# Kernel optimization log

Hardware: AMD Instinct MI355X
Metric: run time of the kernel (lower is better)

## Reference

```python
import jax, jax.numpy as jnp
import numpy as np

B, L, D, H, TOPO = 2, 1024, 1024, 16, 8
Dh = D // H
N_SLOTS = B * L


def _rope_apply(x, cos, sin):
    # x: [B,H,L,Dh]; cos/sin: [B,1,L,Dh//2]
    x1 = x[..., 0::2]
    x2 = x[..., 1::2]
    y1 = x1 * cos - x2 * sin
    y2 = x1 * sin + x2 * cos
    return jnp.stack([y1, y2], axis=-1).reshape(x.shape)


def setup_inputs() -> dict:
    key = jax.random.key(0)
    ks = jax.random.split(key, 6)
    x = jax.random.normal(ks[0], (B, L, D), dtype=jnp.float32)
    topo_active = jax.random.normal(ks[1], (B, L, TOPO), dtype=jnp.float32)
    k_cache = jnp.zeros((1, H, N_SLOTS, Dh), dtype=jnp.float32)
    v_cache = jnp.zeros((1, H, N_SLOTS, Dh), dtype=jnp.float32)
    Wqkv = jax.random.normal(ks[2], (3 * D, D), dtype=jnp.float32) * 0.02
    Wproj = jax.random.normal(ks[3], (D, D), dtype=jnp.float32) * 0.02
    Wfreq = jax.random.normal(ks[4], (Dh // 2, TOPO), dtype=jnp.float32) * 0.02
    # each token (b, pos) writes to physical slot b*L + pos
    slot_mapping = jnp.arange(N_SLOTS, dtype=jnp.int64)
    # paged causal mask: query (b, i) may see slot s iff slot belongs to batch b and pos(s) <= i
    s = jnp.arange(N_SLOTS)
    sb = s // L           # batch owning each slot
    sp = s % L            # position within that sequence
    b_idx = jnp.arange(B)[:, None, None]
    i_idx = jnp.arange(L)[None, :, None]
    block_mask = ((sb[None, None, :] == b_idx) & (sp[None, None, :] <= i_idx))[:, None]  # [B,1,L,S]
    return {"x": x, "topo_active": topo_active, "k_cache": k_cache, "v_cache": v_cache,
            "Wqkv": Wqkv, "Wproj": Wproj, "Wfreq": Wfreq,
            "slot_mapping": slot_mapping, "block_mask": block_mask}


def reference(x, topo_active, k_cache, v_cache, Wqkv, Wproj, Wfreq, slot_mapping, block_mask):
    Bx, Lx, Dx = x.shape
    # qkv projection -> q,k,v [B,H,L,Dh]
    qkv = (x @ Wqkv.T).reshape(Bx, Lx, 3, H, Dh).transpose(2, 0, 3, 1, 4)
    q, k, v = qkv[0], qkv[1], qkv[2]
    # RnRoPE: topo -> per-position frequencies, rotate q and k
    freqs = (topo_active @ Wfreq.T)[:, None]  # [B,1,L,Dh//2]
    cos, sin = jnp.cos(freqs), jnp.sin(freqs)
    q = _rope_apply(q, cos, sin)
    k = _rope_apply(k, cos, sin)
    # commit new k/v into the paged cache via slot_mapping scatter
    k_flat = k.transpose(0, 2, 1, 3).reshape(Bx * Lx, H, Dh).swapaxes(0, 1)  # [H,BL,Dh]
    v_flat = v.transpose(0, 2, 1, 3).reshape(Bx * Lx, H, Dh).swapaxes(0, 1)
    kc = k_cache[0].at[:, slot_mapping].set(k_flat)  # [H,S,Dh]
    vc = v_cache[0].at[:, slot_mapping].set(v_flat)
    # masked (block-sparse) attention over the physical cache
    scale = 1.0 / jnp.sqrt(jnp.float32(Dh))
    scores = jnp.einsum('bhld,hsd->bhls', q, kc) * scale
    scores = jnp.where(block_mask, scores, -jnp.inf)
    p = jax.nn.softmax(scores, axis=-1)
    out = jnp.einsum('bhls,hsd->bhld', p, vc)
    out = out.transpose(0, 2, 1, 3).reshape(Bx, Lx, Dx)
    return out @ Wproj.T
```

## Files before the change

### kernel.cpp

```cpp
#include <hip/hip_runtime.h>
#include <hip/hip_bf16.h>
#include <math.h>

#define H_N 16
#define DH 64
#define LSEQ 1024
#define BATCH 2
#define NSLOT 2048
#define DMODEL 1024

typedef __bf16 bf16x8 __attribute__((ext_vector_type(8)));
typedef __bf16 bf16x4 __attribute__((ext_vector_type(4)));
typedef float f32x4 __attribute__((ext_vector_type(4)));

__global__ __launch_bounds__(256) void k_setup(const float* __restrict__ x,
                                               const float* __restrict__ Wqkv,
                                               const float* __restrict__ Wproj,
                                               const float* __restrict__ topo,
                                               const float* __restrict__ Wfreq,
                                               __bf16* __restrict__ xb,
                                               __bf16* __restrict__ Wqkvb,
                                               __bf16* __restrict__ Wprojb,
                                               float* __restrict__ cosb,
                                               float* __restrict__ sinb) {
    int blk = blockIdx.x;
    if (blk < 6144) {
        const float* in;
        __bf16* out;
        int base;
        if (blk < 2048)      { in = x;     out = xb;     base = blk; }
        else if (blk < 5120) { in = Wqkv;  out = Wqkvb;  base = blk - 2048; }
        else                 { in = Wproj; out = Wprojb; base = blk - 5120; }
        int i = (base * 256 + threadIdx.x) * 4;
        float4 v = *reinterpret_cast<const float4*>(in + i);
        struct B4 { __bf16 a, b, c, d; };
        B4 o{(__bf16)v.x, (__bf16)v.y, (__bf16)v.z, (__bf16)v.w};
        *reinterpret_cast<B4*>(out + i) = o;
    } else {
        int s = (blk - 6144) * 8 + (threadIdx.x >> 5);
        int j = threadIdx.x & 31;
        float f = 0.f;
#pragma unroll
        for (int t = 0; t < 8; ++t) f += topo[s * 8 + t] * Wfreq[j * 8 + t];
        cosb[s * 32 + j] = cosf(f);
        sinb[s * 32 + j] = sinf(f);
    }
}

template <int BM, int BN>
__device__ __forceinline__ void gemm_coreT(const __bf16* __restrict__ A,
                                           const __bf16* __restrict__ Bm,
                                           int K, int m0, int n0,
                                           __bf16* As, __bf16* Bs,
                                           f32x4 acc[BM / 32][BN / 32],
                                           int tid, int wr, int wc, int lane) {
    constexpr int MF = BM / 32, NF = BN / 32;
    const f32x4 z = {0.f, 0.f, 0.f, 0.f};
#pragma unroll
    for (int m = 0; m < MF; ++m)
#pragma unroll
        for (int n = 0; n < NF; ++n) acc[m][n] = z;

    const int l15 = lane & 15, g = lane >> 4;
    const int wv = tid >> 6;
    const int srow = tid >> 3, sslot = tid & 7;
    const int ssrc = (sslot ^ (srow & 7)) * 8;

#pragma unroll
    for (int i = 0; i < MF; ++i) {
        int row = i * 32 + srow;
        __builtin_amdgcn_global_load_lds(
            (const __attribute__((address_space(1))) void*)(A + (size_t)(m0 + row) * K + ssrc),
            (__attribute__((address_space(3))) void*)(As + i * 2048 + wv * 512), 16, 0, 0);
    }
#pragma unroll
    for (int i = 0; i < NF; ++i) {
        int row = i * 32 + srow;
        __builtin_amdgcn_global_load_lds(
            (const __attribute__((address_space(1))) void*)(Bm + (size_t)(n0 + row) * K + ssrc),
            (__attribute__((address_space(3))) void*)(Bs + i * 2048 + wv * 512), 16, 0, 0);
    }
    __syncthreads();

    const int NT = K / 64;
    for (int t = 0; t < NT; ++t) {
        const int cur = t & 1;
        __bf16* Ac = As + cur * (BM * 64);
        __bf16* Bc = Bs + cur * (BN * 64);
        if (t + 1 < NT) {
            const int k0 = (t + 1) * 64;
            __bf16* An = As + (1 - cur) * (BM * 64);
            __bf16* Bn = Bs + (1 - cur) * (BN * 64);
#pragma unroll
            for (int i = 0; i < MF; ++i) {
                int row = i * 32 + srow;
                __builtin_amdgcn_global_load_lds(
                    (const __attribute__((address_space(1))) void*)(A + (size_t)(m0 + row) * K + k0 + ssrc),
                    (__attribute__((address_space(3))) void*)(An + i * 2048 + wv * 512), 16, 0, 0);
            }
#pragma unroll
            for (int i = 0; i < NF; ++i) {
                int row = i * 32 + srow;
                __builtin_amdgcn_global_load_lds(
                    (const __attribute__((address_space(1))) void*)(Bm + (size_t)(n0 + row) * K + k0 + ssrc),
                    (__attribute__((address_space(3))) void*)(Bn + i * 2048 + wv * 512), 16, 0, 0);
            }
        }
        __builtin_amdgcn_s_setprio(1);
#pragma unroll
        for (int kk = 0; kk < 2; ++kk) {
            const int k16 = kk * 4 + g;
            bf16x8 af[MF], bfr[NF];
#pragma unroll
            for (int m = 0; m < MF; ++m) {
                int row = wr * (BM / 2) + m * 16 + l15;
                int slot = k16 ^ (row & 7);
                af[m] = *reinterpret_cast<const bf16x8*>(Ac + row * 64 + slot * 8);
            }
#pragma unroll
            for (int n = 0; n < NF; ++n) {
                int col = wc * (BN / 2) + n * 16 + l15;
                int slot = k16 ^ (col & 7);
                bfr[n] = *reinterpret_cast<const bf16x8*>(Bc + col * 64 + slot * 8);
            }
#pragma unroll
            for (int m = 0; m < MF; ++m)
#pragma unroll
                for (int n = 0; n < NF; ++n)
                    acc[m][n] = __builtin_amdgcn_mfma_f32_16x16x32_bf16(af[m], bfr[n], acc[m][n], 0, 0, 0);
        }
        __builtin_amdgcn_s_setprio(0);
        __syncthreads();
    }
}

__global__ __launch_bounds__(256, 2) void k_qkv_mfma(const __bf16* __restrict__ xb,
                                                     const __bf16* __restrict__ Wb,
                                                     const float* __restrict__ cosb,
                                                     const float* __restrict__ sinb,
                                                     __bf16* __restrict__ Qb,
                                                     __bf16* __restrict__ Kb,
                                                     __bf16* __restrict__ Vtb) {
    __shared__ __bf16 As[2][128 * 64];
    __shared__ __bf16 Bs[2][96 * 64];
    int lin = blockIdx.x;
    int newlin = (lin & 7) * 64 + (lin >> 3);
    const int m0 = (newlin & 15) * 128, n0 = (newlin >> 4) * 96;
    const int tid = threadIdx.x, lane = tid & 63, w = tid >> 6;
    const int wr = w >> 1, wc = w & 1;
    const int l15 = lane & 15, g = lane >> 4;
    f32x4 acc[4][3];
    gemm_coreT<128, 96>(xb, Wb, DMODEL, m0, n0, &As[0][0], &Bs[0][0], acc, tid, wr, wc, lane);

    const int rbase = m0 + wr * 64;
#pragma unroll
    for (int n = 0; n < 3; ++n) {
        int c = n0 + wc * 48 + n * 16 + l15;
        int part = c >> 10, h = (c >> 6) & 15, d = c & 63, jj = d >> 1;
#pragma unroll
        for (int m = 0; m < 4; ++m) {
            int sbase = rbase + m * 16 + g * 4;
            if (part < 2) {
                __bf16* dst = (part == 0) ? Qb : Kb;
#pragma unroll
                for (int j = 0; j < 4; ++j) {
                    int s = sbase + j;
                    float v = acc[m][n][j];
                    float partner = __shfl_xor(v, 1);
                    float cs = cosb[s * 32 + jj], sn = sinb[s * 32 + jj];
                    float outv = (d & 1) ? fmaf(v, cs, partner * sn) : fmaf(v, cs, -partner * sn);
                    dst[((size_t)h * NSLOT + s) * DH + d] = (__bf16)outv;
                }
            } else {
                bf16x4 pk;
#pragma unroll
                for (int j = 0; j < 4; ++j) pk[j] = (__bf16)acc[m][n][j];
                *reinterpret_cast<bf16x4*>(&Vtb[((size_t)h * DH + d) * NSLOT + sbase]) = pk;
            }
        }
    }
}

__global__ __launch_bounds__(256, 2) void k_attn8(const __bf16* __restrict__ Qg,
                                                  const __bf16* __restrict__ Kg,
                                                  const __bf16* __restrict__ Vt,
                                                  __bf16* __restrict__ AO) {
    int lin = blockIdx.x + 16 * (blockIdx.y + 16 * blockIdx.z);
    const int x = lin & 7;
    const int t = lin >> 3;
    const int b = x >> 2;
    const int h = (x & 3) * 4 + (t & 3);
    const int v = t >> 2;
    const int bx = (v < 8) ? v : 23 - v;

    const int tid = threadIdx.x, w = tid >> 6, lane = tid & 63;
    const int l15 = lane & 15, g = lane >> 4;
    const int q0 = bx * 64 + w * 16;

    __shared__ __bf16 Ks[2][64 * 64];
    __shared__ __bf16 Vs[2][64 * 64];
    __shared__ __bf16 P_lds[4][16 * 72];

    const __bf16* Qh = Qg + ((size_t)h * NSLOT + b * LSEQ) * DH;
    const __bf16* Kh = Kg + ((size_t)h * NSLOT + b * LSEQ) * DH;
    const __bf16* Vh = Vt + ((size_t)h * DH) * NSLOT + b * LSEQ;

    bf16x8 qf[2];
#pragma unroll
    for (int g2 = 0; g2 < 2; ++g2)
        qf[g2] = *reinterpret_cast<const bf16x8*>(Qh + (size_t)(q0 + l15) * DH + g2 * 32 + g * 8);

    const f32x4 z = {0.f, 0.f, 0.f, 0.f};
    f32x4 ao[4];
#pragma unroll
    for (int dt = 0; dt < 4; ++dt) ao[dt] = z;
    float lsum[4] = {0.f, 0.f, 0.f, 0.f};

    const int nch = bx + 1;

#pragma unroll
    for (int i = 0; i < 2; ++i) {
        int u = i * 256 + tid;
        int row = u >> 3, slot = u & 7;
        int srcs = slot ^ (row & 7);
        const __bf16* ga = Kh + (size_t)row * DH + srcs * 8;
        const __bf16* gv = Vh + (size_t)row * NSLOT + srcs * 8;
        __builtin_amdgcn_global_load_lds((const __attribute__((address_space(1))) void*)ga,
                                         (__attribute__((address_space(3))) void*)(&Ks[0][u * 8]), 16, 0, 0);
        __builtin_amdgcn_global_load_lds((const __attribute__((address_space(1))) void*)gv,
                                         (__attribute__((address_space(3))) void*)(&Vs[0][u * 8]), 16, 0, 0);
    }
    __syncthreads();

    for (int ch = 0; ch < nch; ++ch) {
        const int cur = ch & 1;
        if (ch + 1 < nch) {
            const int nsp = (ch + 1) * 64;
#pragma unroll
            for (int i = 0; i < 2; ++i) {
                int u = i * 256 + tid;
                int row = u >> 3, slot = u & 7;
                int srcs = slot ^ (row & 7);
                const __bf16* ga = Kh + (size_t)(nsp + row) * DH + srcs * 8;
                const __bf16* gv = Vh + (size_t)row * NSLOT + nsp + srcs * 8;
                __builtin_amdgcn_global_load_lds((const __attribute__((address_space(1))) void*)ga,
                                                 (__attribute__((address_space(3))) void*)(&Ks[1 - cur][u * 8]), 16, 0, 0);
                __builtin_amdgcn_global_load_lds((const __attribute__((address_space(1))) void*)gv,
                                                 (__attribute__((address_space(3))) void*)(&Vs[1 - cur][u * 8]), 16, 0, 0);
            }
        }

        f32x4 s[4];
#pragma unroll
        for (int n = 0; n < 4; ++n) s[n] = z;
        __builtin_amdgcn_s_setprio(1);
#pragma unroll
        for (int g2 = 0; g2 < 2; ++g2) {
#pragma unroll
            for (int n = 0; n < 4; ++n) {
                int r = n * 16 + l15;
                int slot = ((g2 << 2) + g) ^ (r & 7);
                bf16x8 kf = *reinterpret_cast<const bf16x8*>(&Ks[cur][r * 64 + slot * 8]);
                s[n] = __builtin_amdgcn_mfma_f32_16x16x32_bf16(qf[g2], kf, s[n], 0, 0, 0);
            }
        }
        __builtin_amdgcn_s_setprio(0);

        const bool last = (ch == nch - 1);
        const int sp0 = ch * 64;
#pragma unroll
        for (int n = 0; n < 4; ++n) {
            int key = sp0 + n * 16 + l15;
#pragma unroll
            for (int j = 0; j < 4; ++j) {
                float sc = s[n][j] * 0.125f;
                if (last && key > q0 + g * 4 + j) sc = -INFINITY;
                float p = __expf(sc);
                s[n][j] = p;
                lsum[j] += p;
            }
        }

#pragma unroll
        for (int j = 0; j < 4; ++j)
#pragma unroll
            for (int n = 0; n < 4; ++n)
                P_lds[w][(g * 4 + j) * 72 + n * 16 + l15] = (__bf16)s[n][j];

        bf16x8 pf[2];
        pf[0] = *reinterpret_cast<const bf16x8*>(&P_lds[w][l15 * 72 + g * 8]);
        pf[1] = *reinterpret_cast<const bf16x8*>(&P_lds[w][l15 * 72 + 32 + g * 8]);

        __builtin_amdgcn_s_setprio(1);
#pragma unroll
        for (int g2 = 0; g2 < 2; ++g2) {
#pragma unroll
            for (int dt = 0; dt < 4; ++dt) {
                int rv = dt * 16 + l15;
                int slot = ((g2 << 2) + g) ^ (rv & 7);
                bf16x8 vf = *reinterpret_cast<const bf16x8*>(&Vs[cur][rv * 64 + slot * 8]);
                ao[dt] = __builtin_amdgcn_mfma_f32_16x16x32_bf16(pf[g2], vf, ao[dt], 0, 0, 0);
            }
        }
        __builtin_amdgcn_s_setprio(0);

        __syncthreads();
    }

    float lrow[4];
#pragma unroll
    for (int j = 0; j < 4; ++j) {
        float vv = lsum[j];
#pragma unroll
        for (int off = 1; off < 16; off <<= 1) vv += __shfl_xor(vv, off);
        lrow[j] = vv;
    }

#pragma unroll
    for (int dt = 0; dt < 4; ++dt)
#pragma unroll
        for (int j = 0; j < 4; ++j) {
            int q = q0 + g * 4 + j;
            AO[(size_t)(b * LSEQ + q) * DMODEL + h * 64 + dt * 16 + l15] =
                (__bf16)(ao[dt][j] / lrow[j]);
        }
}

__global__ __launch_bounds__(256, 2) void k_proj_mfma(const __bf16* __restrict__ AO,
                                                      const __bf16* __restrict__ Wb,
                                                      float* __restrict__ out) {
    __shared__ __bf16 As[2][64 * 64];
    __shared__ __bf16 Bs[2][64 * 64];
    int lin = blockIdx.x;
    int newlin = (lin & 7) * 64 + (lin >> 3);
    const int m0 = (newlin & 31) * 64, n0 = (newlin >> 5) * 64;
    const int tid = threadIdx.x, lane = tid & 63, w = tid >> 6;
    const int wr = w >> 1, wc = w & 1;
    const int l15 = lane & 15, g = lane >> 4;
    f32x4 acc[2][2];
    gemm_coreT<64, 64>(AO, Wb, DMODEL, m0, n0, &As[0][0], &Bs[0][0], acc, tid, wr, wc, lane);

#pragma unroll
    for (int n = 0; n < 2; ++n) {
        int c = n0 + wc * 32 + n * 16 + l15;
#pragma unroll
        for (int m = 0; m < 2; ++m) {
#pragma unroll
            for (int j = 0; j < 4; ++j) {
                int s = m0 + wr * 32 + m * 16 + g * 4 + j;
                out[(size_t)s * DMODEL + c] = acc[m][n][j];
            }
        }
    }
}

extern "C" void kernel_launch(void* const* d_in, const int* in_sizes, int n_in,
                              void* d_out, int out_size, void* d_ws, size_t ws_size,
                              hipStream_t stream) {
    const float* x     = (const float*)d_in[0];
    const float* topo  = (const float*)d_in[1];
    const float* Wqkv  = (const float*)d_in[4];
    const float* Wproj = (const float*)d_in[5];
    const float* Wfreq = (const float*)d_in[6];
    float* out = (float*)d_out;

    char* wsb = (char*)d_ws;
    __bf16* xb     = (__bf16*)(wsb + 0);
    __bf16* Wqkvb  = (__bf16*)(wsb + (4u << 20));
    __bf16* Wprojb = (__bf16*)(wsb + (10u << 20));
    float*  cosb   = (float*)(wsb + (12u << 20));
    float*  sinb   = (float*)(wsb + (12u << 20) + 262144);
    __bf16* Qb     = (__bf16*)(wsb + (12u << 20) + 524288);
    __bf16* Kb     = (__bf16*)(wsb + (16u << 20) + 524288);
    __bf16* Vtb    = (__bf16*)(wsb + (20u << 20) + 524288);
    __bf16* AO     = (__bf16*)(wsb + (24u << 20) + 524288);

    hipLaunchKernelGGL(k_setup, dim3(6400), dim3(256), 0, stream,
                       x, Wqkv, Wproj, topo, Wfreq, xb, Wqkvb, Wprojb, cosb, sinb);
    hipLaunchKernelGGL(k_qkv_mfma, dim3(512), dim3(256), 0, stream,
                       xb, Wqkvb, cosb, sinb, Qb, Kb, Vtb);
    hipLaunchKernelGGL(k_attn8, dim3(LSEQ / 64, H_N, BATCH), dim3(256), 0, stream,
                       Qb, Kb, Vtb, AO);
    hipLaunchKernelGGL(k_proj_mfma, dim3(512), dim3(256), 0, stream,
                       AO, Wprojb, out);
}
```

Measured before the change: 66.35 us.

## Widen attention key chunks to 128 and use BK=128 for projection GEMM

The attention kernel now processes 128 keys per chunk instead of 64, which halves the number of chunk iterations and barriers. It widens the K/V/P shared-memory tiles and adds an XOR swizzle to the P staging buffer. The shared GEMM core is generalised over a BK template parameter, and the output projection now uses BK=128 so it runs fewer k-steps. The trade-offs are more LDS per block and some wasted masked work on the last chunk for even query blocks, which could lower occupancy.

```diff
diff --git a/kernel.cpp b/kernel.cpp
--- a/kernel.cpp
+++ b/kernel.cpp
@@ -47,7 +47,7 @@
     }
 }
 
-template <int BM, int BN>
+template <int BM, int BN, int BK>
 __device__ __forceinline__ void gemm_coreT(const __bf16* __restrict__ A,
                                            const __bf16* __restrict__ Bm,
                                            int K, int m0, int n0,
@@ -55,6 +55,9 @@
                                            f32x4 acc[BM / 32][BN / 32],
                                            int tid, int wr, int wc, int lane) {
     constexpr int MF = BM / 32, NF = BN / 32;
+    constexpr int SLOTS = BK / 8;
+    constexpr int AIT = BM * SLOTS / 256;
+    constexpr int BIT = BN * SLOTS / 256;
     const f32x4 z = {0.f, 0.f, 0.f, 0.f};
 #pragma unroll
     for (int m = 0; m < MF; ++m)
@@ -63,44 +66,45 @@
 
     const int l15 = lane & 15, g = lane >> 4;
     const int wv = tid >> 6;
-    const int srow = tid >> 3, sslot = tid & 7;
+    const int srow = tid / SLOTS, sslot = tid % SLOTS;
     const int ssrc = (sslot ^ (srow & 7)) * 8;
-
-#pragma unroll
-    for (int i = 0; i < MF; ++i) {
-        int row = i * 32 + srow;
+    constexpr int RPI = 256 / SLOTS;
+
+#pragma unroll
+    for (int i = 0; i < AIT; ++i) {
+        int row = i * RPI + srow;
         __builtin_amdgcn_global_load_lds(
             (const __attribute__((address_space(1))) void*)(A + (size_t)(m0 + row) * K + ssrc),
             (__attribute__((address_space(3))) void*)(As + i * 2048 + wv * 512), 16, 0, 0);
     }
 #pragma unroll
-    for (int i = 0; i < NF; ++i) {
-        int row = i * 32 + srow;
+    for (int i = 0; i < BIT; ++i) {
+        int row = i * RPI + srow;
         __builtin_amdgcn_global_load_lds(
             (const __attribute__((address_space(1))) void*)(Bm + (size_t)(n0 + row) * K + ssrc),
             (__attribute__((address_space(3))) void*)(Bs + i * 2048 + wv * 512), 16, 0, 0);
     }
     __syncthreads();
 
-    const int NT = K / 64;
+    const int NT = K / BK;
     for (int t = 0; t < NT; ++t) {
         const int cur = t & 1;
-        __bf16* Ac = As + cur * (BM * 64);
-        __bf16* Bc = Bs + cur * (BN * 64);
+        __bf16* Ac = As + cur * (BM * BK);
+        __bf16* Bc = Bs + cur * (BN * BK);
         if (t + 1 < NT) {
-            const int k0 = (t + 1) * 64;
-            __bf16* An = As + (1 - cur) * (BM * 64);
-            __bf16* Bn = Bs + (1 - cur) * (BN * 64);
-#pragma unroll
-            for (int i = 0; i < MF; ++i) {
-                int row = i * 32 + srow;
+            const int k0 = (t + 1) * BK;
+            __bf16* An = As + (1 - cur) * (BM * BK);
+            __bf16* Bn = Bs + (1 - cur) * (BN * BK);
+#pragma unroll
+            for (int i = 0; i < AIT; ++i) {
+                int row = i * RPI + srow;
                 __builtin_amdgcn_global_load_lds(
                     (const __attribute__((address_space(1))) void*)(A + (size_t)(m0 + row) * K + k0 + ssrc),
                     (__attribute__((address_space(3))) void*)(An + i * 2048 + wv * 512), 16, 0, 0);
             }
 #pragma unroll
-            for (int i = 0; i < NF; ++i) {
-                int row = i * 32 + srow;
+            for (int i = 0; i < BIT; ++i) {
+                int row = i * RPI + srow;
                 __builtin_amdgcn_global_load_lds(
                     (const __attribute__((address_space(1))) void*)(Bm + (size_t)(n0 + row) * K + k0 + ssrc),
                     (__attribute__((address_space(3))) void*)(Bn + i * 2048 + wv * 512), 16, 0, 0);
@@ -108,20 +112,20 @@
         }
         __builtin_amdgcn_s_setprio(1);
 #pragma unroll
-        for (int kk = 0; kk < 2; ++kk) {
+        for (int kk = 0; kk < BK / 32; ++kk) {
             const int k16 = kk * 4 + g;
             bf16x8 af[MF], bfr[NF];
 #pragma unroll
             for (int m = 0; m < MF; ++m) {
                 int row = wr * (BM / 2) + m * 16 + l15;
                 int slot = k16 ^ (row & 7);
-                af[m] = *reinterpret_cast<const bf16x8*>(Ac + row * 64 + slot * 8);
+                af[m] = *reinterpret_cast<const bf16x8*>(Ac + row * BK + slot * 8);
             }
 #pragma unroll
             for (int n = 0; n < NF; ++n) {
                 int col = wc * (BN / 2) + n * 16 + l15;
                 int slot = k16 ^ (col & 7);
-                bfr[n] = *reinterpret_cast<const bf16x8*>(Bc + col * 64 + slot * 8);
+                bfr[n] = *reinterpret_cast<const bf16x8*>(Bc + col * BK + slot * 8);
             }
 #pragma unroll
             for (int m = 0; m < MF; ++m)
@@ -150,7 +154,7 @@
     const int wr = w >> 1, wc = w & 1;
     const int l15 = lane & 15, g = lane >> 4;
     f32x4 acc[4][3];
-    gemm_coreT<128, 96>(xb, Wb, DMODEL, m0, n0, &As[0][0], &Bs[0][0], acc, tid, wr, wc, lane);
+    gemm_coreT<128, 96, 64>(xb, Wb, DMODEL, m0, n0, &As[0][0], &Bs[0][0], acc, tid, wr, wc, lane);
 
     const int rbase = m0 + wr * 64;
 #pragma unroll
@@ -181,7 +185,7 @@
     }
 }
 
-__global__ __launch_bounds__(256, 2) void k_attn8(const __bf16* __restrict__ Qg,
+__global__ __launch_bounds__(256, 2) void k_attn9(const __bf16* __restrict__ Qg,
                                                   const __bf16* __restrict__ Kg,
                                                   const __bf16* __restrict__ Vt,
                                                   __bf16* __restrict__ AO) {
@@ -197,9 +201,9 @@
     const int l15 = lane & 15, g = lane >> 4;
     const int q0 = bx * 64 + w * 16;
 
-    __shared__ __bf16 Ks[2][64 * 64];
-    __shared__ __bf16 Vs[2][64 * 64];
-    __shared__ __bf16 P_lds[4][16 * 72];
+    __shared__ __bf16 Ks[2][128 * 64];
+    __shared__ __bf16 Vs[2][64 * 128];
+    __shared__ __bf16 P_lds[4][16 * 128];
 
     const __bf16* Qh = Qg + ((size_t)h * NSLOT + b * LSEQ) * DH;
     const __bf16* Kh = Kg + ((size_t)h * NSLOT + b * LSEQ) * DH;
@@ -216,48 +220,56 @@
     for (int dt = 0; dt < 4; ++dt) ao[dt] = z;
     float lsum[4] = {0.f, 0.f, 0.f, 0.f};
 
-    const int nch = bx + 1;
-
-#pragma unroll
-    for (int i = 0; i < 2; ++i) {
+    const int nch = (bx >> 1) + 1;
+
+#pragma unroll
+    for (int i = 0; i < 4; ++i) {
         int u = i * 256 + tid;
-        int row = u >> 3, slot = u & 7;
-        int srcs = slot ^ (row & 7);
-        const __bf16* ga = Kh + (size_t)row * DH + srcs * 8;
-        const __bf16* gv = Vh + (size_t)row * NSLOT + srcs * 8;
-        __builtin_amdgcn_global_load_lds((const __attribute__((address_space(1))) void*)ga,
-                                         (__attribute__((address_space(3))) void*)(&Ks[0][u * 8]), 16, 0, 0);
-        __builtin_amdgcn_global_load_lds((const __attribute__((address_space(1))) void*)gv,
-                                         (__attribute__((address_space(3))) void*)(&Vs[0][u * 8]), 16, 0, 0);
+        {
+            int row = u >> 3, slot = u & 7, srcs = (slot ^ (row & 7)) * 8;
+            __builtin_amdgcn_global_load_lds(
+                (const __attribute__((address_space(1))) void*)(Kh + (size_t)row * DH + srcs),
+                (__attribute__((address_space(3))) void*)(&Ks[0][i * 2048 + (tid >> 6) * 512]), 16, 0, 0);
+        }
+        {
+            int row = u >> 4, slot = u & 15, srcs = (slot ^ (row & 7)) * 8;
+            __builtin_amdgcn_global_load_lds(
+                (const __attribute__((address_space(1))) void*)(Vh + (size_t)row * NSLOT + srcs),
+                (__attribute__((address_space(3))) void*)(&Vs[0][i * 2048 + (tid >> 6) * 512]), 16, 0, 0);
+        }
     }
     __syncthreads();
 
     for (int ch = 0; ch < nch; ++ch) {
         const int cur = ch & 1;
         if (ch + 1 < nch) {
-            const int nsp = (ch + 1) * 64;
-#pragma unroll
-            for (int i = 0; i < 2; ++i) {
+            const int nsp = (ch + 1) * 128;
+#pragma unroll
+            for (int i = 0; i < 4; ++i) {
                 int u = i * 256 + tid;
-                int row = u >> 3, slot = u & 7;
-                int srcs = slot ^ (row & 7);
-                const __bf16* ga = Kh + (size_t)(nsp + row) * DH + srcs * 8;
-                const __bf16* gv = Vh + (size_t)row * NSLOT + nsp + srcs * 8;
-                __builtin_amdgcn_global_load_lds((const __attribute__((address_space(1))) void*)ga,
-                                                 (__attribute__((address_space(3))) void*)(&Ks[1 - cur][u * 8]), 16, 0, 0);
-                __builtin_amdgcn_global_load_lds((const __attribute__((address_space(1))) void*)gv,
-                                                 (__attribute__((address_space(3))) void*)(&Vs[1 - cur][u * 8]), 16, 0, 0);
-            }
-        }
-
-        f32x4 s[4];
-#pragma unroll
-        for (int n = 0; n < 4; ++n) s[n] = z;
+                {
+                    int row = u >> 3, slot = u & 7, srcs = (slot ^ (row & 7)) * 8;
+                    __builtin_amdgcn_global_load_lds(
+                        (const __attribute__((address_space(1))) void*)(Kh + (size_t)(nsp + row) * DH + srcs),
+                        (__attribute__((address_space(3))) void*)(&Ks[1 - cur][i * 2048 + (tid >> 6) * 512]), 16, 0, 0);
+                }
+                {
+                    int row = u >> 4, slot = u & 15, srcs = (slot ^ (row & 7)) * 8;
+                    __builtin_amdgcn_global_load_lds(
+                        (const __attribute__((address_space(1))) void*)(Vh + (size_t)row * NSLOT + nsp + srcs),
+                        (__attribute__((address_space(3))) void*)(&Vs[1 - cur][i * 2048 + (tid >> 6) * 512]), 16, 0, 0);
+                }
+            }
+        }
+
+        f32x4 s[8];
+#pragma unroll
+        for (int n = 0; n < 8; ++n) s[n] = z;
         __builtin_amdgcn_s_setprio(1);
 #pragma unroll
         for (int g2 = 0; g2 < 2; ++g2) {
 #pragma unroll
-            for (int n = 0; n < 4; ++n) {
+            for (int n = 0; n < 8; ++n) {
                 int r = n * 16 + l15;
                 int slot = ((g2 << 2) + g) ^ (r & 7);
                 bf16x8 kf = *reinterpret_cast<const bf16x8*>(&Ks[cur][r * 64 + slot * 8]);
@@ -267,9 +279,9 @@
         __builtin_amdgcn_s_setprio(0);
 
         const bool last = (ch == nch - 1);
-        const int sp0 = ch * 64;
-#pragma unroll
-        for (int n = 0; n < 4; ++n) {
+        const int sp0 = ch * 128;
+#pragma unroll
+        for (int n = 0; n < 8; ++n) {
             int key = sp0 + n * 16 + l15;
 #pragma unroll
             for (int j = 0; j < 4; ++j) {
@@ -282,24 +294,30 @@
         }
 
 #pragma unroll
-        for (int j = 0; j < 4; ++j)
-#pragma unroll
-            for (int n = 0; n < 4; ++n)
-                P_lds[w][(g * 4 + j) * 72 + n * 16 + l15] = (__bf16)s[n][j];
-
-        bf16x8 pf[2];
-        pf[0] = *reinterpret_cast<const bf16x8*>(&P_lds[w][l15 * 72 + g * 8]);
-        pf[1] = *reinterpret_cast<const bf16x8*>(&P_lds[w][l15 * 72 + 32 + g * 8]);
+        for (int j = 0; j < 4; ++j) {
+            int row = g * 4 + j;
+#pragma unroll
+            for (int n = 0; n < 8; ++n) {
+                int slot = n * 2 + (l15 >> 3);
+                P_lds[w][row * 128 + ((slot ^ (row & 7)) << 3) + (l15 & 7)] = (__bf16)s[n][j];
+            }
+        }
+
+        bf16x8 pf[4];
+#pragma unroll
+        for (int kb = 0; kb < 4; ++kb)
+            pf[kb] = *reinterpret_cast<const bf16x8*>(
+                &P_lds[w][l15 * 128 + (((kb << 2) + g) ^ (l15 & 7)) * 8]);
 
         __builtin_amdgcn_s_setprio(1);
 #pragma unroll
-        for (int g2 = 0; g2 < 2; ++g2) {
+        for (int kb = 0; kb < 4; ++kb) {
 #pragma unroll
             for (int dt = 0; dt < 4; ++dt) {
                 int rv = dt * 16 + l15;
-                int slot = ((g2 << 2) + g) ^ (rv & 7);
-                bf16x8 vf = *reinterpret_cast<const bf16x8*>(&Vs[cur][rv * 64 + slot * 8]);
-                ao[dt] = __builtin_amdgcn_mfma_f32_16x16x32_bf16(pf[g2], vf, ao[dt], 0, 0, 0);
+                int slot = ((kb << 2) + g) ^ (rv & 7);
+                bf16x8 vf = *reinterpret_cast<const bf16x8*>(&Vs[cur][rv * 128 + slot * 8]);
+                ao[dt] = __builtin_amdgcn_mfma_f32_16x16x32_bf16(pf[kb], vf, ao[dt], 0, 0, 0);
             }
         }
         __builtin_amdgcn_s_setprio(0);
@@ -329,8 +347,8 @@
 __global__ __launch_bounds__(256, 2) void k_proj_mfma(const __bf16* __restrict__ AO,
                                                       const __bf16* __restrict__ Wb,
                                                       float* __restrict__ out) {
-    __shared__ __bf16 As[2][64 * 64];
-    __shared__ __bf16 Bs[2][64 * 64];
+    __shared__ __bf16 As[2][64 * 128];
+    __shared__ __bf16 Bs[2][64 * 128];
     int lin = blockIdx.x;
     int newlin = (lin & 7) * 64 + (lin >> 3);
     const int m0 = (newlin & 31) * 64, n0 = (newlin >> 5) * 64;
@@ -338,7 +356,7 @@
     const int wr = w >> 1, wc = w & 1;
     const int l15 = lane & 15, g = lane >> 4;
     f32x4 acc[2][2];
-    gemm_coreT<64, 64>(AO, Wb, DMODEL, m0, n0, &As[0][0], &Bs[0][0], acc, tid, wr, wc, lane);
+    gemm_coreT<64, 64, 128>(AO, Wb, DMODEL, m0, n0, &As[0][0], &Bs[0][0], acc, tid, wr, wc, lane);
 
 #pragma unroll
     for (int n = 0; n < 2; ++n) {
@@ -379,7 +397,7 @@
                        x, Wqkv, Wproj, topo, Wfreq, xb, Wqkvb, Wprojb, cosb, sinb);
     hipLaunchKernelGGL(k_qkv_mfma, dim3(512), dim3(256), 0, stream,
                        xb, Wqkvb, cosb, sinb, Qb, Kb, Vtb);
-    hipLaunchKernelGGL(k_attn8, dim3(LSEQ / 64, H_N, BATCH), dim3(256), 0, stream,
+    hipLaunchKernelGGL(k_attn9, dim3(LSEQ / 64, H_N, BATCH), dim3(256), 0, stream,
                        Qb, Kb, Vtb, AO);
     hipLaunchKernelGGL(k_proj_mfma, dim3(512), dim3(256), 0, stream,
                        AO, Wprojb, out);
```

Measured after the change: 62.07 us. 6.5% less time.
